# Kernel tuning notes

Measured on AMD Instinct MI355X. Metric: run time of the kernel, lower is better.

The kernel has to match this reference:

```python
import jax, jax.numpy as jnp
import numpy as np
import math

N, E, C, NB, NEL, NG = 8192, 131072, 64, 8, 4, 16
R_MAX, AVG_NEI, P_CUT, NL, SH = 5.0, 16.0, 6, 2, 16


def _sph(u):
    # real spherical harmonics l=0..3, component normalization (sum_m Y_lm^2 = 2l+1 on unit sphere)
    x, y, z = u[:, 0], u[:, 1], u[:, 2]
    s3, s15, s5 = math.sqrt(3.0), math.sqrt(15.0), math.sqrt(5.0)
    s105, s7 = math.sqrt(105.0), math.sqrt(7.0)
    c35, c21 = math.sqrt(35.0 / 8.0), math.sqrt(21.0 / 8.0)
    Y = [jnp.ones_like(x),
         s3 * x, s3 * y, s3 * z,
         s15 * x * y, s15 * y * z, 0.5 * s5 * (3 * z * z - 1), s15 * x * z, 0.5 * s15 * (x * x - y * y),
         c35 * y * (3 * x * x - y * y), s105 * x * y * z, c21 * y * (5 * z * z - 1),
         0.5 * s7 * (5 * z ** 3 - 3 * z), c21 * x * (5 * z * z - 1),
         0.5 * s105 * z * (x * x - y * y), c35 * x * (x * x - 3 * y * y)]
    return jnp.stack(Y, axis=-1)  # [E,16]


def _bessel(r):
    k = jnp.arange(1, NB + 1, dtype=r.dtype)
    return math.sqrt(2.0 / R_MAX) * jnp.sin(k * jnp.pi * r[:, None] / R_MAX) / r[:, None]


def _poly_cutoff(r):
    p = float(P_CUT)
    x = r / R_MAX
    f = (1.0 - 0.5 * (p + 1) * (p + 2) * x ** p + p * (p + 2) * x ** (p + 1)
         - 0.5 * p * (p + 1) * x ** (p + 2))
    return f * (x < 1.0)


def setup_inputs() -> dict:
    key = jax.random.key(0)
    ks = jax.random.split(key, 16)
    sc = lambda fan: 1.0 / math.sqrt(fan)
    return {
        "pos": 2.0 * jax.random.normal(ks[0], (N, 3), jnp.float32),
        "atom_types": jax.random.randint(ks[1], (N,), 0, NEL),
        "edge_index": jax.random.randint(ks[2], (2, E), 0, N),
        "batch": jnp.sort(jax.random.randint(ks[3], (N,), 0, NG)),
        "W_embed": jax.random.normal(ks[4], (NEL, C), jnp.float32),
        "W_r1": sc(NB) * jax.random.normal(ks[5], (NL, NB, 64), jnp.float32),
        "W_r2": sc(64) * jax.random.normal(ks[6], (NL, 64, 64), jnp.float32),
        "W_r3": sc(64) * jax.random.normal(ks[7], (NL, 64, C), jnp.float32),
        "W_sc": sc(C) * jax.random.normal(ks[8], (NL, NEL, C, C), jnp.float32),
        "w_prod": 0.5 * jax.random.normal(ks[9], (NL, NEL, 4), jnp.float32),
        "w_ro0": sc(C) * jax.random.normal(ks[10], (C,), jnp.float32),
        "W_ro1a": sc(C) * jax.random.normal(ks[11], (C, 16), jnp.float32),
        "w_ro1b": sc(16) * jax.random.normal(ks[12], (16,), jnp.float32),
    }


def reference(pos, atom_types, edge_index, batch, W_embed, W_r1, W_r2, W_r3,
              W_sc, w_prod, w_ro0, W_ro1a, w_ro1b):
    src, dst = edge_index[0], edge_index[1]
    vec = pos[dst] - pos[src]                      # [E,3]
    r = jnp.sqrt(jnp.sum(vec * vec, -1) + 1e-12)   # [E]
    Y = _sph(vec / r[:, None])                     # [E,SH]
    edge_feats = _bessel(r) * _poly_cutoff(r)[:, None]  # [E,NB]
    h = W_embed[atom_types]                        # one-hot @ W == lookup, [N,C]
    energies = [jnp.zeros((NG,), pos.dtype)]       # pair_repulsion disabled
    for i in range(NL):
        Rw = jax.nn.silu(edge_feats @ W_r1[i])
        Rw = jax.nn.silu(Rw @ W_r2[i])
        Rw = Rw @ W_r3[i]                          # radial MLP weights [E,C]
        # gather-TP-scatter: message [E,C,SH] -> node A [N,C,SH]
        m = (Rw * h[src])[:, :, None] * Y[:, None, :]
        A = jax.ops.segment_sum(m.reshape(E, C * SH), dst,
                                num_segments=N).reshape(N, C, SH) / AVG_NEI
        sc_feat = jnp.einsum('nc,ncd->nd', h, W_sc[i][atom_types])  # element-dep skip
        inv = jnp.stack([A[:, :, 0],
                         jnp.sum(A[:, :, 1:4] ** 2, -1),
                         jnp.sum(A[:, :, 4:9] ** 2, -1),
                         jnp.sum(A[:, :, 9:16] ** 2, -1)], axis=-1)  # [N,C,4]
        h = jnp.einsum('ncj,nj->nc', inv, w_prod[i][atom_types]) + sc_feat
        if i < NL - 1:
            e_node = h @ w_ro0                     # linear readout
        else:
            e_node = jax.nn.silu(h @ W_ro1a) @ w_ro1b  # gated MLP readout
        energies.append(jax.ops.segment_sum(e_node, batch, num_segments=NG))
    contributions = jnp.stack(energies, -1)        # [NG, NL+1]
    return jnp.sum(contributions, -1)              # total energy per graph
```

## Files before the change

kernel.cpp:

```cpp
#include <hip/hip_runtime.h>
#include <hip/hip_bf16.h>
#include <math.h>

#define N_NODES 8192
#define N_EDGES 131072
#define NGRP 16
#define NLAY 2
#define NELM 4
#define SLOT_STRIDE 64
#define N_SLOTS (N_NODES*SLOT_STRIDE)
constexpr float INV_AVG = 1.0f / 16.0f;
constexpr float PI_F = 3.14159265358979323846f;

#define CV_EMB   0
#define CV_SC    256
#define CV_PROD  33024
#define CV_RO0   33056
#define CV_RO1A  33120
#define CV_RO1B  34144
#define CV_SC0T  34160
#define CVT_WORK 34160
#define CVT_N    34416

#define SWZ_PER_L 10240
#define SWZ_N     20480

#define B_GEOM 512
#define B_CVT  134
#define B_SWZ  80
#define SETUP_GRID (B_GEOM + B_CVT + B_SWZ + 1)

typedef __hip_bfloat16 bf16;
typedef __attribute__((ext_vector_type(8))) short bf16x8;
typedef __attribute__((ext_vector_type(4))) float f32x4;

__device__ __forceinline__ float silu_f(float x){ return x / (1.0f + __expf(-x)); }
__device__ __forceinline__ float bfbits2f(unsigned short u){
  return __uint_as_float(((unsigned)u) << 16);
}
__device__ __forceinline__ void unpack2(unsigned u, float& lo, float& hi){
  lo = __uint_as_float(u << 16);
  hi = __uint_as_float(u & 0xffff0000u);
}
__device__ __forceinline__ short f2bs(float v){
  union { bf16 b; short s; } u; u.b = __float2bfloat16(v); return u.s;
}
__device__ __forceinline__ float ldf(const void* p, int i, int flag){
  if (flag) return bfbits2f(((const unsigned short*)p)[i]);
  return ((const float*)p)[i];
}
__device__ __forceinline__ int detect_fl(const void* pos){
  int lane = threadIdx.x & 63;
  const unsigned short* u = (const unsigned short*)pos;
  float va = bfbits2f(u[2*lane]), vb = bfbits2f(u[2*lane+1]);
  bool bad = !(fabsf(va) <= 1000.0f) || !(fabsf(vb) <= 1000.0f);
  return (__ballot(bad) == 0ull) ? 1 : 0;
}
__device__ __forceinline__ void WSYNC(){ __builtin_amdgcn_wave_barrier(); }

__device__ __forceinline__ void gl_lds4(const void* g, void* l){
  __builtin_amdgcn_global_load_lds(
      (const __attribute__((address_space(1))) unsigned*)g,
      (__attribute__((address_space(3))) unsigned*)l, 4, 0, 0);
}

__global__ void k_setup(const void* __restrict__ pos, const int* __restrict__ types,
                        const int* __restrict__ ei,
                        const void* __restrict__ Wemb, const void* __restrict__ Wsc,
                        const void* __restrict__ wprod, const void* __restrict__ wro0,
                        const void* __restrict__ Wro1a, const void* __restrict__ wro1b,
                        const void* __restrict__ Wr1, const void* __restrict__ Wr2,
                        const void* __restrict__ Wr3,
                        int* __restrict__ cursor, int* __restrict__ sslot,
                        unsigned char* __restrict__ tsl,
                        unsigned short* __restrict__ Yb, float* __restrict__ rbuf,
                        float* __restrict__ cv, short* __restrict__ swz){
  int b = blockIdx.x, tix = threadIdx.x;
  int fl = detect_fl(pos);
  if (b < B_GEOM){
    int e = b*256 + tix;
    int s = ei[e], d = ei[N_EDGES + e];
    int slot = (d << 6) + atomicAdd(&cursor[d], 1);
    sslot[slot] = s;
    tsl[slot] = (unsigned char)types[s];
    float vx = ldf(pos, d*3+0, fl) - ldf(pos, s*3+0, fl);
    float vy = ldf(pos, d*3+1, fl) - ldf(pos, s*3+1, fl);
    float vz = ldf(pos, d*3+2, fl) - ldf(pos, s*3+2, fl);
    float r = sqrtf(vx*vx + vy*vy + vz*vz + 1e-12f);
    float ir = 1.0f / r;
    float x = vx*ir, y = vy*ir, z = vz*ir;
    const float s3 = 1.7320508075688772f, s15 = 3.872983346207417f, s5 = 2.23606797749979f;
    const float s105 = 10.246950765959598f, s7 = 2.6457513110645907f;
    const float c35 = 2.091650066335189f, c21 = 1.6201851746019651f;
    float x2 = x*x, y2 = y*y, z2 = z*z;
    float ys[16] = {
      1.0f, s3*x, s3*y, s3*z,
      s15*x*y, s15*y*z, 0.5f*s5*(3.0f*z2-1.0f), s15*x*z,
      0.5f*s15*(x2-y2), c35*y*(3.0f*x2-y2), s105*x*y*z, c21*y*(5.0f*z2-1.0f),
      0.5f*s7*(5.0f*z2*z-3.0f*z), c21*x*(5.0f*z2-1.0f), 0.5f*s105*z*(x2-y2),
      c35*x*(x2-3.0f*y2) };
    union { bf16 bb[16]; uint4 u[2]; } pk;
#pragma unroll
    for (int k = 0; k < 16; k++) pk.bb[k] = __float2bfloat16(ys[k]);
    uint4* yp = (uint4*)(Yb + (size_t)slot*16);
    yp[0] = pk.u[0];
    yp[1] = pk.u[1];
    rbuf[slot] = r;
    return;
  }
  if (b < B_GEOM + B_CVT){
    int i = (b - B_GEOM)*256 + tix;
    if (i < 256)  { cv[CV_EMB + i] = ldf(Wemb, i, fl); return; }
    if (i < 33024){ int j=i-256;   cv[CV_SC  + j] = ldf(Wsc,  j, fl); return; }
    if (i < 33056){ int j=i-33024; cv[CV_PROD+ j] = ldf(wprod,j, fl); return; }
    if (i < 33120){ int j=i-33056; cv[CV_RO0 + j] = ldf(wro0, j, fl); return; }
    if (i < 34144){ int j=i-33120; cv[CV_RO1A+ j] = ldf(Wro1a,j, fl); return; }
    if (i < CVT_WORK){ int j=i-34144; cv[CV_RO1B+ j] = ldf(wro1b,j, fl); return; }
    return;
  }
  if (b < B_GEOM + B_CVT + B_SWZ){
    int i = (b - B_GEOM - B_CVT)*256 + tix;
    int l = i / SWZ_PER_L, w = i % SWZ_PER_L;
    float v;
    if (w < 2048){
      int t = w >> 9, q = (w >> 7) & 3, n = (w >> 3) & 15, j = w & 7;
      int k = q*8 + j;
      v = (k < 8) ? ldf(Wr1, l*512 + k*64 + t*16 + n, fl) : 0.0f;
    } else if (w < 6144){
      int w2 = w - 2048;
      int nt = w2 >> 10, kt = (w2 >> 9) & 1, q = (w2 >> 7) & 3, n = (w2 >> 3) & 15, j = w2 & 7;
      int k = kt*32 + q*8 + j;
      v = ldf(Wr2, l*4096 + k*64 + nt*16 + n, fl);
    } else {
      int w3 = w - 6144;
      int nt = w3 >> 10, kt = (w3 >> 9) & 1, q = (w3 >> 7) & 3, n = (w3 >> 3) & 15, j = w3 & 7;
      int k = kt*32 + q*8 + j;
      v = ldf(Wr3, l*4096 + k*64 + nt*16 + n, fl);
    }
    swz[i] = f2bs(v);
    return;
  }
  {
    int ty = tix >> 6, d = tix & 63;
    float s = 0.0f;
#pragma unroll 8
    for (int c = 0; c < 64; c++)
      s += ldf(Wemb, ty*64 + c, fl) * ldf(Wsc, ty*4096 + c*64 + d, fl);
    cv[CV_SC0T + tix] = s;
  }
}

#define ROWS 72
template<int LAYER_KIND>
__global__ void __launch_bounds__(64) k_gu(const short* __restrict__ sw,
        const float* __restrict__ rbuf, const unsigned char* __restrict__ tsl,
        const int* __restrict__ sslot, const float* __restrict__ h_old,
        float* __restrict__ h_new, const unsigned short* __restrict__ Yb,
        const int* __restrict__ cursor, const int* __restrict__ types,
        const float* __restrict__ Wsc, const float* __restrict__ wprod,
        const float* __restrict__ wemb, const float* __restrict__ sc0t,
        const float* __restrict__ wro0,
        const float* __restrict__ Wro1a, const float* __restrict__ wro1b,
        const int* __restrict__ batch, float* __restrict__ ene2){
  __shared__ __align__(16) short A_[16*ROWS];
  __shared__ __align__(16) float hS[LAYER_KIND ? 16 : 1][64];
  __shared__ __align__(16) unsigned short yS[16][16];
  __shared__ float hn_l[64];
  int lane = threadIdx.x;
  int q = lane >> 4, nn = lane & 15;
  int n = blockIdx.x;
  int beg = n << 6;
  int end = beg + cursor[n];
  short* A = A_;

  const bf16x8* S1 = (const bf16x8*)(sw);
  const bf16x8* S2 = (const bf16x8*)(sw + 2048);
  const bf16x8* S3 = (const bf16x8*)(sw + 6144);

  float e0=0.f, e1=0.f, e2=0.f, e3=0.f;
  if (LAYER_KIND == 0){
    e0 = wemb[lane]; e1 = wemb[64+lane]; e2 = wemb[128+lane]; e3 = wemb[192+lane];
  }

  float acc[16];
#pragma unroll
  for (int s = 0; s < 16; s++) acc[s] = 0.0f;

  for (int cb = beg; cb < end; cb += 16){
    int cnt = min(16, end - cb);
    WSYNC();
    const char* ysrc = (const char*)Yb + (size_t)cb*32 + lane*4;
    gl_lds4(ysrc,       &yS[0][0]);
    gl_lds4(ysrc + 256, &yS[8][0]);
    int tv = 0;
    if (LAYER_KIND == 0){
      tv = (int)tsl[cb + nn];
    } else {
      int sv = sslot[cb + nn];
      for (int i = 0; i < cnt; i++){
        int src = __builtin_amdgcn_readlane(sv, i);
        gl_lds4(h_old + (size_t)src*64 + lane, &hS[i][0]);
      }
    }
    {
      float r = rbuf[cb + nn];
      float xc = r * 0.2f;
      float f = 0.0f;
      if (xc < 1.0f){
        float x3 = xc*xc*xc, x6 = x3*x3, x7 = x6*xc, x8 = x7*xc;
        f = 1.0f - 28.0f*x6 + 48.0f*x7 - 21.0f*x8;
      }
      float bs = 0.6324555320336759f * f / r;
      float t0 = PI_F * r * 0.2f;
      bf16x8 af1 = {0,0,0,0,0,0,0,0};
      if (q == 0){
#pragma unroll
        for (int j = 0; j < 8; j++) af1[j] = f2bs(bs * __sinf((float)(j+1) * t0));
      }
      f32x4 macc[4];
#pragma unroll
      for (int t = 0; t < 4; t++){
        bf16x8 b = S1[t*64 + q*16 + nn];
        f32x4 z = {0.f,0.f,0.f,0.f};
        macc[t] = __builtin_amdgcn_mfma_f32_16x16x32_bf16(af1, b, z, 0, 0, 0);
      }
#pragma unroll
      for (int t = 0; t < 4; t++)
#pragma unroll
        for (int rg = 0; rg < 4; rg++)
          A[(q*4+rg)*ROWS + t*16 + nn] = f2bs(silu_f(macc[t][rg]));
      WSYNC();
      bf16x8 a0 = *(const bf16x8*)&A[nn*ROWS + 0*32 + q*8];
      bf16x8 a1 = *(const bf16x8*)&A[nn*ROWS + 1*32 + q*8];
      WSYNC();
#pragma unroll
      for (int t = 0; t < 4; t++){
        f32x4 z = {0.f,0.f,0.f,0.f};
        bf16x8 b0 = S2[t*128 + 0*64 + q*16 + nn];
        bf16x8 b1 = S2[t*128 + 1*64 + q*16 + nn];
        z = __builtin_amdgcn_mfma_f32_16x16x32_bf16(a0, b0, z, 0, 0, 0);
        z = __builtin_amdgcn_mfma_f32_16x16x32_bf16(a1, b1, z, 0, 0, 0);
        macc[t] = z;
      }
#pragma unroll
      for (int t = 0; t < 4; t++)
#pragma unroll
        for (int rg = 0; rg < 4; rg++)
          A[(q*4+rg)*ROWS + t*16 + nn] = f2bs(silu_f(macc[t][rg]));
      WSYNC();
      a0 = *(const bf16x8*)&A[nn*ROWS + 0*32 + q*8];
      a1 = *(const bf16x8*)&A[nn*ROWS + 1*32 + q*8];
      WSYNC();
#pragma unroll
      for (int t = 0; t < 4; t++){
        f32x4 z = {0.f,0.f,0.f,0.f};
        bf16x8 b0 = S3[t*128 + 0*64 + q*16 + nn];
        bf16x8 b1 = S3[t*128 + 1*64 + q*16 + nn];
        z = __builtin_amdgcn_mfma_f32_16x16x32_bf16(a0, b0, z, 0, 0, 0);
        z = __builtin_amdgcn_mfma_f32_16x16x32_bf16(a1, b1, z, 0, 0, 0);
        macc[t] = z;
      }
#pragma unroll
      for (int t = 0; t < 4; t++)
#pragma unroll
        for (int rg = 0; rg < 4; rg++)
          A[(q*4+rg)*ROWS + t*16 + nn] = f2bs(macc[t][rg]);
      WSYNC();
    }
    asm volatile("s_waitcnt vmcnt(0)" ::: "memory");
    __builtin_amdgcn_sched_barrier(0);
    for (int i = 0; i < cnt; i++){
      float rw = bfbits2f((unsigned short)A[i*ROWS + lane]);
      float hv;
      if (LAYER_KIND == 0){
        int ty = __builtin_amdgcn_readlane(tv, i);
        hv = (ty & 2) ? ((ty & 1) ? e3 : e2) : ((ty & 1) ? e1 : e0);
      } else {
        hv = hS[i][lane];
      }
      float g = rw * hv;
      const uint4* yq = (const uint4*)&yS[i][0];
      uint4 ya = yq[0], yb = yq[1];
      float lo, hi;
      unpack2(ya.x, lo, hi); acc[0]  += g*lo; acc[1]  += g*hi;
      unpack2(ya.y, lo, hi); acc[2]  += g*lo; acc[3]  += g*hi;
      unpack2(ya.z, lo, hi); acc[4]  += g*lo; acc[5]  += g*hi;
      unpack2(ya.w, lo, hi); acc[6]  += g*lo; acc[7]  += g*hi;
      unpack2(yb.x, lo, hi); acc[8]  += g*lo; acc[9]  += g*hi;
      unpack2(yb.y, lo, hi); acc[10] += g*lo; acc[11] += g*hi;
      unpack2(yb.z, lo, hi); acc[12] += g*lo; acc[13] += g*hi;
      unpack2(yb.w, lo, hi); acc[14] += g*lo; acc[15] += g*hi;
    }
  }
#pragma unroll
  for (int s = 0; s < 16; s++) acc[s] *= INV_AVG;

  int ty = __builtin_amdgcn_readfirstlane(types[n]);
  float sc;
  if (LAYER_KIND == 0){
    sc = sc0t[ty*64 + lane];
  } else {
    const float* Ws = Wsc + (size_t)ty*4096;
    const float* hrow = h_old + (size_t)n*64;
    float sc0 = 0.f, sc1 = 0.f, sc2 = 0.f, sc3 = 0.f;
#pragma unroll
    for (int c = 0; c < 64; c += 4){
      sc0 += hrow[c+0] * Ws[(c+0)*64 + lane];
      sc1 += hrow[c+1] * Ws[(c+1)*64 + lane];
      sc2 += hrow[c+2] * Ws[(c+2)*64 + lane];
      sc3 += hrow[c+3] * Ws[(c+3)*64 + lane];
    }
    sc = (sc0 + sc1) + (sc2 + sc3);
  }

  float inv0 = acc[0];
  float inv1 = acc[1]*acc[1] + acc[2]*acc[2] + acc[3]*acc[3];
  float inv2 = acc[4]*acc[4] + acc[5]*acc[5] + acc[6]*acc[6] + acc[7]*acc[7]
             + acc[8]*acc[8];
  float inv3 = acc[9]*acc[9] + acc[10]*acc[10] + acc[11]*acc[11] + acc[12]*acc[12]
             + acc[13]*acc[13] + acc[14]*acc[14] + acc[15]*acc[15];
  const float* wp = wprod + ty*4;
  float hn = inv0*wp[0] + inv1*wp[1] + inv2*wp[2] + inv3*wp[3] + sc;
  if (LAYER_KIND == 0)
    h_new[(size_t)n*64 + lane] = hn;

  float ev;
  if (LAYER_KIND == 0){
    float p = hn * wro0[lane];
#pragma unroll
    for (int off = 32; off >= 1; off >>= 1) p += __shfl_xor(p, off, 64);
    ev = p;
  } else {
    hn_l[lane] = hn;
    WSYNC();
    int j = lane & 15;
    float pj = 0.0f;
#pragma unroll
    for (int c = 0; c < 64; c++)
      pj += hn_l[c] * Wro1a[c*16 + j];
    float evj = silu_f(pj) * wro1b[j];
    evj += __shfl_xor(evj, 8, 64);
    evj += __shfl_xor(evj, 4, 64);
    evj += __shfl_xor(evj, 2, 64);
    evj += __shfl_xor(evj, 1, 64);
    ev = evj;
  }
  if (lane == 0) atomicAdd(&ene2[(n & 7)*NGRP + batch[n]], ev);
}

__global__ void k_out(const float* __restrict__ ene2, const void* __restrict__ pos,
                      void* __restrict__ out){
  int fl = detect_fl(pos);
  int t = threadIdx.x;
  if (t < NGRP){
    float v = 0.0f;
#pragma unroll
    for (int k = 0; k < 8; k++) v += ene2[k*NGRP + t];
    if (fl) ((bf16*)out)[t] = __float2bfloat16(v);
    else    ((float*)out)[t] = v;
  }
}

static inline size_t rup(size_t x){ return (x + 255) & ~(size_t)255; }

extern "C" void kernel_launch(void* const* d_in, const int* in_sizes, int n_in,
                              void* d_out, int out_size, void* d_ws, size_t ws_size,
                              hipStream_t stream) {
  const void* pos   = d_in[0];
  const int*  types = (const int*)d_in[1];
  const int*  ei    = (const int*)d_in[2];
  const int*  batch = (const int*)d_in[3];
  const void* Wemb  = d_in[4];
  const void* Wr1   = d_in[5];
  const void* Wr2   = d_in[6];
  const void* Wr3   = d_in[7];
  const void* Wsc   = d_in[8];
  const void* wprod = d_in[9];
  const void* wro0  = d_in[10];
  const void* Wro1a = d_in[11];
  const void* wro1b = d_in[12];

  char* w = (char*)d_ws;
  float* ene2     = (float*)w; w += 512;
  int*   cursor   = (int*)  w; w += rup((size_t)N_NODES*4);
  float* cv       = (float*)w; w += rup((size_t)CVT_N*4);
  short* swz      = (short*)w; w += rup((size_t)SWZ_N*2);
  int*   sslot    = (int*)  w; w += rup((size_t)N_SLOTS*4);
  unsigned char* tsl = (unsigned char*)w; w += rup((size_t)N_SLOTS);
  float* hbuf     = (float*)w; w += rup((size_t)N_NODES*64*4);
  float* rbuf     = (float*)w; w += rup((size_t)N_SLOTS*4);
  unsigned short* Yb = (unsigned short*)w; w += rup((size_t)N_SLOTS*16*2);
  w += 4096;

  hipMemsetAsync(ene2, 0, 512 + (size_t)N_NODES*4, stream);

  k_setup<<<SETUP_GRID, 256, 0, stream>>>(pos, types, ei,
      Wemb, Wsc, wprod, wro0, Wro1a, wro1b, Wr1, Wr2, Wr3,
      cursor, sslot, tsl, Yb, rbuf, cv, swz);

  k_gu<0><<<N_NODES, 64, 0, stream>>>(swz, rbuf, tsl, sslot,
      hbuf , hbuf , Yb, cursor, types,
      cv + CV_SC, cv + CV_PROD, cv + CV_EMB, cv + CV_SC0T,
      cv + CV_RO0, cv + CV_RO1A, cv + CV_RO1B, batch, ene2);
  k_gu<1><<<N_NODES, 64, 0, stream>>>(swz + SWZ_PER_L, rbuf, tsl, sslot,
      hbuf , hbuf , Yb, cursor, types,
      cv + CV_SC + (size_t)NELM*4096, cv + CV_PROD + NELM*4, cv + CV_EMB,
      cv + CV_SC0T, cv + CV_RO0, cv + CV_RO1A, cv + CV_RO1B, batch, ene2);

  k_out<<<1, 64, 0, stream>>>(ene2, pos, d_out);
}
```

Measured before the change: 176.2 us.

## Store Y by edge id with slot indirection and prefetch next chunk metadata

Spherical harmonics are now stored by original edge index instead of the destination slot, so the setup writes are coalesced. The node kernel gathers them through a new eslot indirection array, 32 bytes per edge. The main loop becomes a do-while that prefetches the next chunk's slot metadata (edge id, source, type, radius) while computing the current chunk. Layer 1 now always issues 16 h_old row loads, masked to valid indices, removing the variable-count loop. The cost is an extra index array, scattered Y reads in the hot kernel, and wasted loads for partial chunks.

```diff
diff --git a/kernel.cpp b/kernel.cpp
--- a/kernel.cpp
+++ b/kernel.cpp
@@ -72,7 +72,7 @@
                         const void* __restrict__ Wr1, const void* __restrict__ Wr2,
                         const void* __restrict__ Wr3,
                         int* __restrict__ cursor, int* __restrict__ sslot,
-                        unsigned char* __restrict__ tsl,
+                        unsigned char* __restrict__ tsl, int* __restrict__ eslot,
                         unsigned short* __restrict__ Yb, float* __restrict__ rbuf,
                         float* __restrict__ cv, short* __restrict__ swz){
   int b = blockIdx.x, tix = threadIdx.x;
@@ -83,6 +83,7 @@
     int slot = (d << 6) + atomicAdd(&cursor[d], 1);
     sslot[slot] = s;
     tsl[slot] = (unsigned char)types[s];
+    eslot[slot] = e;
     float vx = ldf(pos, d*3+0, fl) - ldf(pos, s*3+0, fl);
     float vy = ldf(pos, d*3+1, fl) - ldf(pos, s*3+1, fl);
     float vz = ldf(pos, d*3+2, fl) - ldf(pos, s*3+2, fl);
@@ -102,7 +103,7 @@
     union { bf16 bb[16]; uint4 u[2]; } pk;
 #pragma unroll
     for (int k = 0; k < 16; k++) pk.bb[k] = __float2bfloat16(ys[k]);
-    uint4* yp = (uint4*)(Yb + (size_t)slot*16);
+    uint4* yp = (uint4*)(Yb + (size_t)e*16);
     yp[0] = pk.u[0];
     yp[1] = pk.u[1];
     rbuf[slot] = r;
@@ -154,7 +155,8 @@
 template<int LAYER_KIND>
 __global__ void __launch_bounds__(64) k_gu(const short* __restrict__ sw,
         const float* __restrict__ rbuf, const unsigned char* __restrict__ tsl,
-        const int* __restrict__ sslot, const float* __restrict__ h_old,
+        const int* __restrict__ sslot, const int* __restrict__ eslot,
+        const float* __restrict__ h_old,
         float* __restrict__ h_new, const unsigned short* __restrict__ Yb,
         const int* __restrict__ cursor, const int* __restrict__ types,
         const float* __restrict__ Wsc, const float* __restrict__ wprod,
@@ -170,7 +172,6 @@
   int q = lane >> 4, nn = lane & 15;
   int n = blockIdx.x;
   int beg = n << 6;
-  int end = beg + cursor[n];
   short* A = A_;
 
   const bf16x8* S1 = (const bf16x8*)(sw);
@@ -182,28 +183,41 @@
     e0 = wemb[lane]; e1 = wemb[64+lane]; e2 = wemb[128+lane]; e3 = wemb[192+lane];
   }
 
+  int dcnt = cursor[n];
+  int ev  = eslot[beg + nn];
+  int sv  = (LAYER_KIND == 1) ? sslot[beg + nn] : 0;
+  int tvp = (LAYER_KIND == 0) ? (int)tsl[beg + nn] : 0;
+  float rv = rbuf[beg + nn];
+  int end = beg + dcnt;
+
   float acc[16];
 #pragma unroll
   for (int s = 0; s < 16; s++) acc[s] = 0.0f;
 
-  for (int cb = beg; cb < end; cb += 16){
-    int cnt = min(16, end - cb);
+  int cb = beg;
+  do {
     WSYNC();
-    const char* ysrc = (const char*)Yb + (size_t)cb*32 + lane*4;
-    gl_lds4(ysrc,       &yS[0][0]);
-    gl_lds4(ysrc + 256, &yS[8][0]);
-    int tv = 0;
-    if (LAYER_KIND == 0){
-      tv = (int)tsl[cb + nn];
-    } else {
-      int sv = sslot[cb + nn];
-      for (int i = 0; i < cnt; i++){
-        int src = __builtin_amdgcn_readlane(sv, i);
+    {
+      int er0 = __shfl(ev, (lane >> 3)) & (N_EDGES - 1);
+      gl_lds4((const char*)Yb + (size_t)er0*32 + (lane & 7)*4, &yS[0][0]);
+      int er1 = __shfl(ev, 8 + (lane >> 3)) & (N_EDGES - 1);
+      gl_lds4((const char*)Yb + (size_t)er1*32 + (lane & 7)*4, &yS[8][0]);
+    }
+    int tv = tvp;
+    if (LAYER_KIND == 1){
+#pragma unroll
+      for (int i = 0; i < 16; i++){
+        int src = __builtin_amdgcn_readlane(sv, i) & (N_NODES - 1);
         gl_lds4(h_old + (size_t)src*64 + lane, &hS[i][0]);
       }
     }
+    int nx = min(cb + 16 + nn, N_SLOTS - 1);
+    int ev_n = eslot[nx];
+    int sv_n = (LAYER_KIND == 1) ? sslot[nx] : 0;
+    int tv_n = (LAYER_KIND == 0) ? (int)tsl[nx] : 0;
+    float rv_n = rbuf[nx];
     {
-      float r = rbuf[cb + nn];
+      float r = rv;
       float xc = r * 0.2f;
       float f = 0.0f;
       if (xc < 1.0f){
@@ -269,6 +283,7 @@
     }
     asm volatile("s_waitcnt vmcnt(0)" ::: "memory");
     __builtin_amdgcn_sched_barrier(0);
+    int cnt = min(16, end - cb);
     for (int i = 0; i < cnt; i++){
       float rw = bfbits2f((unsigned short)A[i*ROWS + lane]);
       float hv;
@@ -291,7 +306,9 @@
       unpack2(yb.z, lo, hi); acc[12] += g*lo; acc[13] += g*hi;
       unpack2(yb.w, lo, hi); acc[14] += g*lo; acc[15] += g*hi;
     }
-  }
+    ev = ev_n; sv = sv_n; tvp = tv_n; rv = rv_n;
+    cb += 16;
+  } while (cb < end);
 #pragma unroll
   for (int s = 0; s < 16; s++) acc[s] *= INV_AVG;
 
@@ -324,12 +341,12 @@
   if (LAYER_KIND == 0)
     h_new[(size_t)n*64 + lane] = hn;
 
-  float ev;
+  float ev_;
   if (LAYER_KIND == 0){
     float p = hn * wro0[lane];
 #pragma unroll
     for (int off = 32; off >= 1; off >>= 1) p += __shfl_xor(p, off, 64);
-    ev = p;
+    ev_ = p;
   } else {
     hn_l[lane] = hn;
     WSYNC();
@@ -343,9 +360,9 @@
     evj += __shfl_xor(evj, 4, 64);
     evj += __shfl_xor(evj, 2, 64);
     evj += __shfl_xor(evj, 1, 64);
-    ev = evj;
-  }
-  if (lane == 0) atomicAdd(&ene2[(n & 7)*NGRP + batch[n]], ev);
+    ev_ = evj;
+  }
+  if (lane == 0) atomicAdd(&ene2[(n & 7)*NGRP + batch[n]], ev_);
 }
 
 __global__ void k_out(const float* __restrict__ ene2, const void* __restrict__ pos,
@@ -385,24 +402,25 @@
   int*   cursor   = (int*)  w; w += rup((size_t)N_NODES*4);
   float* cv       = (float*)w; w += rup((size_t)CVT_N*4);
   short* swz      = (short*)w; w += rup((size_t)SWZ_N*2);
-  int*   sslot    = (int*)  w; w += rup((size_t)N_SLOTS*4);
-  unsigned char* tsl = (unsigned char*)w; w += rup((size_t)N_SLOTS);
+  int*   sslot    = (int*)  w; w += rup((size_t)N_SLOTS*4) + 256;
+  unsigned char* tsl = (unsigned char*)w; w += rup((size_t)N_SLOTS) + 256;
+  int*   eslot    = (int*)  w; w += rup((size_t)N_SLOTS*4) + 256;
   float* hbuf     = (float*)w; w += rup((size_t)N_NODES*64*4);
-  float* rbuf     = (float*)w; w += rup((size_t)N_SLOTS*4);
-  unsigned short* Yb = (unsigned short*)w; w += rup((size_t)N_SLOTS*16*2);
+  float* rbuf     = (float*)w; w += rup((size_t)N_SLOTS*4) + 256;
+  unsigned short* Yb = (unsigned short*)w; w += rup((size_t)N_EDGES*16*2);
   w += 4096;
 
   hipMemsetAsync(ene2, 0, 512 + (size_t)N_NODES*4, stream);
 
   k_setup<<<SETUP_GRID, 256, 0, stream>>>(pos, types, ei,
       Wemb, Wsc, wprod, wro0, Wro1a, wro1b, Wr1, Wr2, Wr3,
-      cursor, sslot, tsl, Yb, rbuf, cv, swz);
-
-  k_gu<0><<<N_NODES, 64, 0, stream>>>(swz, rbuf, tsl, sslot,
+      cursor, sslot, tsl, eslot, Yb, rbuf, cv, swz);
+
+  k_gu<0><<<N_NODES, 64, 0, stream>>>(swz, rbuf, tsl, sslot, eslot,
       hbuf , hbuf , Yb, cursor, types,
       cv + CV_SC, cv + CV_PROD, cv + CV_EMB, cv + CV_SC0T,
       cv + CV_RO0, cv + CV_RO1A, cv + CV_RO1B, batch, ene2);
-  k_gu<1><<<N_NODES, 64, 0, stream>>>(swz + SWZ_PER_L, rbuf, tsl, sslot,
+  k_gu<1><<<N_NODES, 64, 0, stream>>>(swz + SWZ_PER_L, rbuf, tsl, sslot, eslot,
       hbuf , hbuf , Yb, cursor, types,
       cv + CV_SC + (size_t)NELM*4096, cv + CV_PROD + NELM*4, cv + CV_EMB,
       cv + CV_SC0T, cv + CV_RO0, cv + CV_RO1A, cv + CV_RO1B, batch, ene2);
```

Measured after the change: 168.5 us. -4.3%, faster.
